# Kernel tuning notes

Measured on AMD Instinct MI355X. Metric: run time of the kernel, lower is better.

The kernel has to match this reference:

```python
import jax, jax.numpy as jnp
import numpy as np

NB_ACTIONS = 64
EPS = 1e-7  # K.epsilon()
B = 32768
NB_ELEMS = (NB_ACTIONS * NB_ACTIONS + NB_ACTIONS) // 2  # 2080

# static tril index pattern (constants, computed once)
_TRIL_ROWS, _TRIL_COLS = np.tril_indices(NB_ACTIONS)
_IS_DIAG = jnp.asarray(_TRIL_ROWS == _TRIL_COLS)
_TRIL_ROWS = jnp.asarray(_TRIL_ROWS)
_TRIL_COLS = jnp.asarray(_TRIL_COLS)


def setup_inputs() -> dict:
    key = jax.random.key(0)
    k1, k2, k3 = jax.random.split(key, 3)
    L_flat = jax.random.normal(k1, (B, NB_ELEMS), dtype=jnp.float32)
    mu = jax.random.normal(k2, (B, NB_ACTIONS), dtype=jnp.float32)
    a = jax.random.normal(k3, (B, NB_ACTIONS), dtype=jnp.float32)
    return {"L_flat": L_flat, "mu": mu, "a": a}


def reference(L_flat, mu, a):
    # diag entries -> exp(x) + eps, off-diag kept raw (matches TF 'full' path)
    vals = jnp.where(_IS_DIAG, jnp.exp(L_flat) + EPS, L_flat)  # [B, nb_elems]
    bsz = L_flat.shape[0]
    L = jnp.zeros((bsz, NB_ACTIONS, NB_ACTIONS), dtype=L_flat.dtype)
    L = L.at[:, _TRIL_ROWS, _TRIL_COLS].set(vals)  # lower-triangular [B, n, n]
    P = jnp.einsum('bik,bjk->bij', L, L)  # L @ L^T
    d = a - mu  # [B, n]
    quad = jnp.einsum('bi,bij,bj->b', d, P, d)
    A = -0.5 * quad[:, None]  # [B, 1]
    return A
```

## Files before the change

### kernel.cpp

```cpp
#include <hip/hip_runtime.h>

#define NB 64
#define NB_ELEMS 2080
#define EPS 1e-7f

__global__ __launch_bounds__(256) void naf_quad_kernel(
    const float* __restrict__ L_flat,
    const float* __restrict__ mu,
    const float* __restrict__ a,
    float* __restrict__ out, int batch)
{
    const int lane = threadIdx.x & 63;
    const int wave = threadIdx.x >> 6;
    const int b = (blockIdx.x << 2) + wave;
    if (b >= batch) return;

    const float* __restrict__ Lb = L_flat + (size_t)b * NB_ELEMS;

    const float d = a[(size_t)b * NB + lane] - mu[(size_t)b * NB + lane];

    float yacc[4] = {0.f, 0.f, 0.f, 0.f};

#pragma unroll
    for (int i = 0; i < NB; ++i) {
        const int base = i * (i + 1) / 2;
        float x = Lb[base + lane];
        float v = (lane == i) ? (__expf(x) + EPS) : x;
        v = (lane <= i) ? v : 0.f;
        const float di = __shfl(d, i);
        yacc[i & 3] = fmaf(v, di, yacc[i & 3]);
    }

    const float y = (yacc[0] + yacc[1]) + (yacc[2] + yacc[3]);
    float q = y * y;

#pragma unroll
    for (int off = 32; off > 0; off >>= 1)
        q += __shfl_xor(q, off);

    if (lane == 0) out[b] = -0.5f * q;
}

extern "C" void kernel_launch(void* const* d_in, const int* in_sizes, int n_in,
                              void* d_out, int out_size, void* d_ws, size_t ws_size,
                              hipStream_t stream) {
    const float* L_flat = (const float*)d_in[0];
    const float* mu     = (const float*)d_in[1];
    const float* a      = (const float*)d_in[2];
    float* out = (float*)d_out;

    const int batch  = in_sizes[0] / NB_ELEMS;
    const int blocks = (batch + 3) / 4;
    naf_quad_kernel<<<blocks, 256, 0, stream>>>(L_flat, mu, a, out, batch);
}
```

Measured before the change: 371.5 us.

## Stage per-row L triangle in LDS via float4 loads before compute

Each wave copies its row's 2080-float packed triangle into shared memory with coalesced float4 loads, then reads the triangle rows from LDS. The diagonal exp is computed once per lane instead of inside the loop, and d is broadcast from LDS instead of through shuffles. This replaces 64 misaligned scalar global loads per lane with vectorized loads. In exchange it uses about 33KB of LDS per block, which may limit occupancy, and adds a block barrier.

```diff
diff --git a/kernel.cpp b/kernel.cpp
--- a/kernel.cpp
+++ b/kernel.cpp
@@ -3,6 +3,7 @@
 #define NB 64
 #define NB_ELEMS 2080
 #define EPS 1e-7f
+#define TRI(i) ((i) * ((i) + 1) / 2)
 
 __global__ __launch_bounds__(256) void naf_quad_kernel(
     const float* __restrict__ L_flat,
@@ -10,35 +11,64 @@
     const float* __restrict__ a,
     float* __restrict__ out, int batch)
 {
+    __shared__ float sL[4 * NB_ELEMS];
+    __shared__ float sd[4 * NB];
+
     const int lane = threadIdx.x & 63;
     const int wave = threadIdx.x >> 6;
     const int b = (blockIdx.x << 2) + wave;
-    if (b >= batch) return;
+    const bool active = b < batch;
 
-    const float* __restrict__ Lb = L_flat + (size_t)b * NB_ELEMS;
+    float* __restrict__ wL = sL + wave * NB_ELEMS;
+    float* __restrict__ wd = sd + wave * NB;
 
-    const float d = a[(size_t)b * NB + lane] - mu[(size_t)b * NB + lane];
+    if (active) {
+        const float4* __restrict__ Lb4 =
+            (const float4*)(L_flat + (size_t)b * NB_ELEMS);
+        float4* __restrict__ wL4 = (float4*)wL;
+#pragma unroll
+        for (int k = 0; k < 8; ++k)
+            wL4[k * 64 + lane] = Lb4[k * 64 + lane];
+        if (lane < 8)
+            wL4[512 + lane] = Lb4[512 + lane];
 
-    float yacc[4] = {0.f, 0.f, 0.f, 0.f};
+        const float dv = a[(size_t)b * NB + lane] - mu[(size_t)b * NB + lane];
+        wd[lane] = dv;
+    }
+
+    __syncthreads();
+
+    if (active) {
+        const float dv = wd[lane];
+
+        const float ldiag = __expf(wL[TRI(lane) + lane]) + EPS;
+        float y0 = ldiag * dv;
+        float y1 = 0.f;
 
 #pragma unroll
-    for (int i = 0; i < NB; ++i) {
-        const int base = i * (i + 1) / 2;
-        float x = Lb[base + lane];
-        float v = (lane == i) ? (__expf(x) + EPS) : x;
-        v = (lane <= i) ? v : 0.f;
-        const float di = __shfl(d, i);
-        yacc[i & 3] = fmaf(v, di, yacc[i & 3]);
-    }
+        for (int i0 = 0; i0 < NB; i0 += 4) {
+            const float4 d4 = *(const float4*)(wd + i0);
+            const float dc[4] = {d4.x, d4.y, d4.z, d4.w};
+#pragma unroll
+            for (int k = 0; k < 4; ++k) {
+                const int i = i0 + k;
+                if (i == 0) continue;
+                const float x = wL[TRI(i) + lane];
+                const float v = (lane < i) ? x : 0.f;
+                if (k & 1) y1 = fmaf(v, dc[k], y1);
+                else       y0 = fmaf(v, dc[k], y0);
+            }
+        }
 
-    const float y = (yacc[0] + yacc[1]) + (yacc[2] + yacc[3]);
-    float q = y * y;
+        float q = y0 + y1;
+        q = q * q;
 
 #pragma unroll
-    for (int off = 32; off > 0; off >>= 1)
-        q += __shfl_xor(q, off);
+        for (int off = 32; off > 0; off >>= 1)
+            q += __shfl_xor(q, off);
 
-    if (lane == 0) out[b] = -0.5f * q;
+        if (lane == 0) out[b] = -0.5f * q;
+    }
 }
 
 extern "C" void kernel_launch(void* const* d_in, const int* in_sizes, int n_in,
```

Measured after the change: 369.0 us. Within noise of the previous version (-0.7%).
